# Kernel optimization log

Measured on AMD Instinct MI355X. Metric: run time of the kernel, lower is better.

Reference implementation:

```python
import jax, jax.numpy as jnp
import numpy as np
jax.config.update("jax_enable_x64", True)

N_ITER = 5
B, N = 64, 128

_C1 = jnp.uint64(0x9E3779B97F4A7C15)
_C2 = jnp.uint64(0xBF58476D1CE4E5B9)
_C3 = jnp.uint64(0x94D049BB133111EB)
_SALT = jnp.uint64(0xD1B54A32D192ED03)


def _mix(x):
    # splitmix64 finalizer: a bijection on uint64 -> preserves label equality classes
    z = x + _C1
    z = (z ^ (z >> jnp.uint64(30))) * _C2
    z = (z ^ (z >> jnp.uint64(27))) * _C3
    return z ^ (z >> jnp.uint64(31))


def setup_inputs() -> dict:
    key = jax.random.key(0)
    k1, k2 = jax.random.split(key)
    u = jax.random.uniform(k1, (B, N, N))
    adj = jnp.where(u < 0.06, 1.0, 0.0).astype(jnp.float32)
    adj = jnp.maximum(adj, jnp.transpose(adj, (0, 2, 1)))  # symmetric
    eye = jnp.eye(N, dtype=jnp.float32)
    adj = adj * (1.0 - eye)  # no self loops
    labels = jax.random.randint(k2, (B, N), 0, 10, dtype=jnp.int32)
    return {"adj": adj, "labels": labels}


def _kernel_contrib(h):
    # h: [B, N] uint64 labels. K[i,j] = #{(u,v): label_u == label_v}
    L = h.reshape(-1)                                   # [T]
    eq = (L[:, None] == L[None, :]).astype(jnp.float32)  # [T, T]
    return eq.reshape(B, N, B, N).sum(axis=(1, 3))       # [B, B]


def reference(adj, labels):
    adj_u = (adj > 0.5).astype(jnp.uint64)        # [B, N, N]
    h = _mix(labels.astype(jnp.uint64))           # initial labels (bijective relabel)
    K = _kernel_contrib(h)
    for _ in range(N_ITER):
        # commutative multiset hash of neighbor labels
        nsum = jnp.einsum('bij,bj->bi', adj_u, _mix(h ^ _SALT))
        # combine own label with neighbor multiset -> WL relabel
        h = _mix(_mix(h) + nsum)
        K = K + _kernel_contrib(h)
    d = jnp.sqrt(jnp.diag(K))
    return K / (d[:, None] * d[None, :])
```

## Files before the change

### kernel.cpp

```cpp
#include <hip/hip_runtime.h>

typedef unsigned long long u64;
typedef unsigned int u32;

#define NB 64
#define NN 128
#define NITER 5
#define NGEN 6
#define SALT 0xD1B54A32D192ED03ULL
#define NPAIR_OFF (NB*(NB-1)/2)
#define TSLOTS 256

__device__ __forceinline__ u64 mix64(u64 x) {
    u64 z = x + 0x9E3779B97F4A7C15ULL;
    z = (z ^ (z >> 30)) * 0xBF58476D1CE4E5B9ULL;
    z = (z ^ (z >> 27)) * 0x94D049BB133111EBULL;
    return z ^ (z >> 31);
}

__device__ __forceinline__ void tab_insert(ulonglong2* tab, u64 key) {
    u32 s = (u32)key & (TSLOTS - 1);
    for (;;) {
        u64 old = atomicCAS((unsigned long long*)&tab[s].x, 0ULL, key);
        if (old == 0ULL || old == key) {
            atomicAdd((unsigned long long*)&tab[s].y, 1ULL);
            return;
        }
        s = (s + 1) & (TSLOTS - 1);
    }
}

__global__ __launch_bounds__(512) void wl_propagate(const float* __restrict__ adj,
                                                    const int* __restrict__ labels,
                                                    u64* __restrict__ hgen,
                                                    ulonglong2* __restrict__ tabg,
                                                    float* __restrict__ Kdiag,
                                                    float* __restrict__ out) {
    const int b = blockIdx.x;
    const int t = threadIdx.x;
    const int wave = t >> 6;
    const int lane = t & 63;

    __shared__ u64 bits_sh[NN][2];
    __shared__ u64 h_sh[NN];
    __shared__ u64 g_sh[NN];
    __shared__ u64 psum[4][NN];
    __shared__ ulonglong2 tab[NGEN][TSLOTS];
    __shared__ u32 part[8];

    const float* abase = adj + (size_t)b * NN * NN;
    #pragma unroll
    for (int k = 0; k < 16; ++k) {
        const int row = wave * 16 + k;
        const float* arow = abase + (size_t)row * NN;
        u64 m0 = __ballot(arow[lane] > 0.5f);
        u64 m1 = __ballot(arow[64 + lane] > 0.5f);
        if (lane == 0) { bits_sh[row][0] = m0; bits_sh[row][1] = m1; }
    }

    {
        ulonglong2* tf = &tab[0][0];
        #pragma unroll
        for (int k = 0; k < 3; ++k) tf[t + 512 * k] = make_ulonglong2(0ULL, 0ULL);
    }

    if (t < NN) {
        u64 h = mix64((u64)(unsigned)labels[b * NN + t]);
        h_sh[t] = h;
        hgen[(size_t)b * (NGEN * NN) + t] = h;
    }
    __syncthreads();

    if (t < NN) tab_insert(tab[0], h_sh[t]);

    for (int it = 0; it < NITER; ++it) {
        if (t < NN) g_sh[t] = mix64(h_sh[t] ^ SALT);
        __syncthreads();
        {
            const int i = t & 127;
            const int q = t >> 7;
            u32 m = (u32)(bits_sh[i][q >> 1] >> ((q & 1) * 32));
            const u64* gp = g_sh + q * 32;
            u64 s = 0;
            while (m) {
                int j = __builtin_ctz(m);
                m &= m - 1;
                s += gp[j];
            }
            psum[q][i] = s;
        }
        __syncthreads();
        if (t < NN) {
            u64 hn = mix64(mix64(h_sh[t]) + psum[0][t] + psum[1][t] + psum[2][t] + psum[3][t]);
            h_sh[t] = hn;
            hgen[(size_t)b * (NGEN * NN) + (it + 1) * NN + t] = hn;
            tab_insert(tab[it + 1], hn);
        }
        __syncthreads();
    }

    {
        const ulonglong2* tf = &tab[0][0];
        ulonglong2* tg = tabg + (size_t)b * (NGEN * TSLOTS);
        u32 acc = 0;
        #pragma unroll
        for (int k = 0; k < 3; ++k) {
            const ulonglong2 v = tf[t + 512 * k];
            tg[t + 512 * k] = v;
            const u32 c = (u32)v.y;
            acc += c * c;
        }
        #pragma unroll
        for (int off = 32; off > 0; off >>= 1) acc += __shfl_down(acc, off);
        if (lane == 0) part[wave] = acc;
        __syncthreads();
        if (t == 0) {
            u32 d = 0;
            #pragma unroll
            for (int w = 0; w < 8; ++w) d += part[w];
            Kdiag[b] = (float)d;
            out[b * NB + b] = 1.0f;
        }
    }
}

__global__ __launch_bounds__(256) void wl_pairs(const u64* __restrict__ hgen,
                                                const ulonglong2* __restrict__ tabg,
                                                const float* __restrict__ Kdiag,
                                                float* __restrict__ out) {
    const int p = blockIdx.x;
    int b1 = (int)((1.0f + sqrtf(1.0f + 8.0f * (float)p)) * 0.5f);
    while (b1 * (b1 - 1) / 2 > p) --b1;
    while ((b1 + 1) * b1 / 2 <= p) ++b1;
    const int b2 = p - b1 * (b1 - 1) / 2;

    const int t = threadIdx.x;
    __shared__ ulonglong2 tab[NGEN * TSLOTS];

    {
        const ulonglong2* src = tabg + (size_t)b2 * (NGEN * TSLOTS);
        #pragma unroll
        for (int k = 0; k < 6; ++k) tab[t + 256 * k] = src[t + 256 * k];
    }
    __syncthreads();

    u32 cnt = 0;
    const u64* abase = hgen + (size_t)b1 * (NGEN * NN);
    #pragma unroll
    for (int k = 0; k < 3; ++k) {
        const int idx = t + 256 * k;
        const u64 a = abase[idx];
        const ulonglong2* tg = tab + (idx >> 7) * TSLOTS;
        u32 s = (u32)a & (TSLOTS - 1);
        for (;;) {
            const ulonglong2 v = tg[s];
            if (v.x == a) { cnt += (u32)v.y; break; }
            if (v.x == 0ULL) break;
            s = (s + 1) & (TSLOTS - 1);
        }
    }

    #pragma unroll
    for (int off = 32; off > 0; off >>= 1) cnt += __shfl_down(cnt, off);
    __shared__ u32 part[4];
    if ((t & 63) == 0) part[t >> 6] = cnt;
    __syncthreads();
    if (t == 0) {
        const float v = (float)(part[0] + part[1] + part[2] + part[3])
                      / (sqrtf(Kdiag[b1]) * sqrtf(Kdiag[b2]));
        out[b1 * NB + b2] = v;
        out[b2 * NB + b1] = v;
    }
}

extern "C" void kernel_launch(void* const* d_in, const int* in_sizes, int n_in,
                              void* d_out, int out_size, void* d_ws, size_t ws_size,
                              hipStream_t stream) {
    const float* adj   = (const float*)d_in[0];
    const int*  labels = (const int*)d_in[1];
    float* out = (float*)d_out;

    char* ws = (char*)d_ws;
    u64*        hgen  = (u64*)ws;
    float*      Kdiag = (float*)(ws + 448 * 1024);
    ulonglong2* tabg  = (ulonglong2*)(ws + 512 * 1024);

    wl_propagate<<<NB, 512, 0, stream>>>(adj, labels, hgen, tabg, Kdiag, out);
    wl_pairs<<<NPAIR_OFF, 256, 0, stream>>>(hgen, tabg, Kdiag, out);
}
```

Before: 32.33 us.

## Split hash-table building into separate kernel and shrink per-block state

Hash-table construction moves out of the propagation kernel into a new wl_tables kernel that runs one block per (graph, generation), so tables are built in parallel instead of serially inside each iteration. The propagation kernel now keeps the adjacency bitmask and the label in registers, using float4 loads instead of ballots, and drops one barrier per iteration. Table layout becomes separate key and 32-bit count arrays, so the pair kernel copies less data into shared memory. The cost is an extra kernel launch, a global round-trip for hgen, and a Kdiag accumulated with atomics.

After: 27.96 us. 1.16x faster.

```diff
diff --git a/kernel.cpp b/kernel.cpp
--- a/kernel.cpp
+++ b/kernel.cpp
@@ -18,115 +18,100 @@
     return z ^ (z >> 31);
 }
 
-__device__ __forceinline__ void tab_insert(ulonglong2* tab, u64 key) {
-    u32 s = (u32)key & (TSLOTS - 1);
-    for (;;) {
-        u64 old = atomicCAS((unsigned long long*)&tab[s].x, 0ULL, key);
-        if (old == 0ULL || old == key) {
-            atomicAdd((unsigned long long*)&tab[s].y, 1ULL);
-            return;
-        }
-        s = (s + 1) & (TSLOTS - 1);
-    }
-}
-
-__global__ __launch_bounds__(512) void wl_propagate(const float* __restrict__ adj,
-                                                    const int* __restrict__ labels,
-                                                    u64* __restrict__ hgen,
-                                                    ulonglong2* __restrict__ tabg,
-                                                    float* __restrict__ Kdiag,
-                                                    float* __restrict__ out) {
+__global__ __launch_bounds__(512) void wl_iter(const float* __restrict__ adj,
+                                               const int* __restrict__ labels,
+                                               u64* __restrict__ hgen,
+                                               u32* __restrict__ KdiagU,
+                                               float* __restrict__ out) {
     const int b = blockIdx.x;
     const int t = threadIdx.x;
-    const int wave = t >> 6;
-    const int lane = t & 63;
+    const int u = t & 127;
+    const int q = t >> 7;
 
-    __shared__ u64 bits_sh[NN][2];
-    __shared__ u64 h_sh[NN];
-    __shared__ u64 g_sh[NN];
-    __shared__ u64 psum[4][NN];
-    __shared__ ulonglong2 tab[NGEN][TSLOTS];
-    __shared__ u32 part[8];
+    __shared__ u64 gsh[NN];
+    __shared__ u64 psum[3][NN];
 
-    const float* abase = adj + (size_t)b * NN * NN;
+    const float* rowp = adj + ((size_t)b * NN + u) * NN + q * 32;
+    u32 m = 0;
     #pragma unroll
-    for (int k = 0; k < 16; ++k) {
-        const int row = wave * 16 + k;
-        const float* arow = abase + (size_t)row * NN;
-        u64 m0 = __ballot(arow[lane] > 0.5f);
-        u64 m1 = __ballot(arow[64 + lane] > 0.5f);
-        if (lane == 0) { bits_sh[row][0] = m0; bits_sh[row][1] = m1; }
+    for (int k = 0; k < 8; ++k) {
+        const float4 v = *(const float4*)(rowp + 4 * k);
+        m |= (v.x > 0.5f ? 1u : 0u) << (4 * k);
+        m |= (v.y > 0.5f ? 1u : 0u) << (4 * k + 1);
+        m |= (v.z > 0.5f ? 1u : 0u) << (4 * k + 2);
+        m |= (v.w > 0.5f ? 1u : 0u) << (4 * k + 3);
     }
 
-    {
-        ulonglong2* tf = &tab[0][0];
-        #pragma unroll
-        for (int k = 0; k < 3; ++k) tf[t + 512 * k] = make_ulonglong2(0ULL, 0ULL);
+    u64 h = 0;
+    if (q == 0) {
+        h = mix64((u64)(u32)labels[b * NN + u]);
+        hgen[((size_t)b * NGEN) * NN + u] = h;
+        if (u == 0) out[b * NB + b] = 1.0f;
+        if (u == 1) KdiagU[b] = 0u;
     }
 
-    if (t < NN) {
-        u64 h = mix64((u64)(unsigned)labels[b * NN + t]);
-        h_sh[t] = h;
-        hgen[(size_t)b * (NGEN * NN) + t] = h;
-    }
-    __syncthreads();
-
-    if (t < NN) tab_insert(tab[0], h_sh[t]);
-
     for (int it = 0; it < NITER; ++it) {
-        if (t < NN) g_sh[t] = mix64(h_sh[t] ^ SALT);
+        if (q == 0) gsh[u] = mix64(h ^ SALT);
         __syncthreads();
+        u64 s = 0;
         {
-            const int i = t & 127;
-            const int q = t >> 7;
-            u32 m = (u32)(bits_sh[i][q >> 1] >> ((q & 1) * 32));
-            const u64* gp = g_sh + q * 32;
-            u64 s = 0;
-            while (m) {
-                int j = __builtin_ctz(m);
-                m &= m - 1;
-                s += gp[j];
-            }
-            psum[q][i] = s;
+            u32 mm = m;
+            const u64* gp = gsh + q * 32;
+            while (mm) { int j = __builtin_ctz(mm); mm &= mm - 1; s += gp[j]; }
         }
+        if (q) psum[q - 1][u] = s;
         __syncthreads();
-        if (t < NN) {
-            u64 hn = mix64(mix64(h_sh[t]) + psum[0][t] + psum[1][t] + psum[2][t] + psum[3][t]);
-            h_sh[t] = hn;
-            hgen[(size_t)b * (NGEN * NN) + (it + 1) * NN + t] = hn;
-            tab_insert(tab[it + 1], hn);
-        }
-        __syncthreads();
-    }
-
-    {
-        const ulonglong2* tf = &tab[0][0];
-        ulonglong2* tg = tabg + (size_t)b * (NGEN * TSLOTS);
-        u32 acc = 0;
-        #pragma unroll
-        for (int k = 0; k < 3; ++k) {
-            const ulonglong2 v = tf[t + 512 * k];
-            tg[t + 512 * k] = v;
-            const u32 c = (u32)v.y;
-            acc += c * c;
-        }
-        #pragma unroll
-        for (int off = 32; off > 0; off >>= 1) acc += __shfl_down(acc, off);
-        if (lane == 0) part[wave] = acc;
-        __syncthreads();
-        if (t == 0) {
-            u32 d = 0;
-            #pragma unroll
-            for (int w = 0; w < 8; ++w) d += part[w];
-            Kdiag[b] = (float)d;
-            out[b * NB + b] = 1.0f;
+        if (q == 0) {
+            h = mix64(mix64(h) + s + psum[0][u] + psum[1][u] + psum[2][u]);
+            hgen[((size_t)b * NGEN + (it + 1)) * NN + u] = h;
         }
     }
 }
 
+__global__ __launch_bounds__(128) void wl_tables(const u64* __restrict__ hgen,
+                                                 u64* __restrict__ keysg,
+                                                 u32* __restrict__ cntsg,
+                                                 u32* __restrict__ KdiagU) {
+    const int bg = blockIdx.x;
+    const int t = threadIdx.x;
+
+    __shared__ u64 keys[TSLOTS];
+    __shared__ u32 cnts[TSLOTS];
+    keys[t] = 0ULL; keys[t + 128] = 0ULL;
+    cnts[t] = 0u;   cnts[t + 128] = 0u;
+    __syncthreads();
+
+    const u64 h = hgen[(size_t)bg * NN + t];
+    u32 s = (u32)h & (TSLOTS - 1);
+    for (;;) {
+        u64 old = atomicCAS((unsigned long long*)&keys[s], 0ULL, h);
+        if (old == 0ULL || old == h) { atomicAdd(&cnts[s], 1u); break; }
+        s = (s + 1) & (TSLOTS - 1);
+    }
+    __syncthreads();
+
+    u32 acc;
+    {
+        const u64 k0 = keys[t], k1 = keys[t + 128];
+        const u32 c0 = cnts[t], c1 = cnts[t + 128];
+        keysg[(size_t)bg * TSLOTS + t]       = k0;
+        keysg[(size_t)bg * TSLOTS + t + 128] = k1;
+        cntsg[(size_t)bg * TSLOTS + t]       = c0;
+        cntsg[(size_t)bg * TSLOTS + t + 128] = c1;
+        acc = c0 * c0 + c1 * c1;
+    }
+    #pragma unroll
+    for (int off = 32; off > 0; off >>= 1) acc += __shfl_down(acc, off);
+    __shared__ u32 part[2];
+    if ((t & 63) == 0) part[t >> 6] = acc;
+    __syncthreads();
+    if (t == 0) atomicAdd(&KdiagU[bg / NGEN], part[0] + part[1]);
+}
+
 __global__ __launch_bounds__(256) void wl_pairs(const u64* __restrict__ hgen,
-                                                const ulonglong2* __restrict__ tabg,
-                                                const float* __restrict__ Kdiag,
+                                                const u64* __restrict__ keysg,
+                                                const u32* __restrict__ cntsg,
+                                                const u32* __restrict__ KdiagU,
                                                 float* __restrict__ out) {
     const int p = blockIdx.x;
     int b1 = (int)((1.0f + sqrtf(1.0f + 8.0f * (float)p)) * 0.5f);
@@ -135,39 +120,50 @@
     const int b2 = p - b1 * (b1 - 1) / 2;
 
     const int t = threadIdx.x;
-    __shared__ ulonglong2 tab[NGEN * TSLOTS];
+    __shared__ u64 keys[NGEN * TSLOTS];
+    __shared__ u32 cnts[NGEN * TSLOTS];
 
     {
-        const ulonglong2* src = tabg + (size_t)b2 * (NGEN * TSLOTS);
+        const ulonglong2* src = (const ulonglong2*)(keysg + (size_t)b2 * NGEN * TSLOTS);
+        ulonglong2* dst = (ulonglong2*)keys;
         #pragma unroll
-        for (int k = 0; k < 6; ++k) tab[t + 256 * k] = src[t + 256 * k];
+        for (int k = 0; k < 3; ++k) dst[t + 256 * k] = src[t + 256 * k];
+    }
+    {
+        const uint4* src = (const uint4*)(cntsg + (size_t)b2 * NGEN * TSLOTS);
+        uint4* dst = (uint4*)cnts;
+        #pragma unroll
+        for (int k = 0; k < 2; ++k) {
+            const int idx = t + 256 * k;
+            if (idx < 384) dst[idx] = src[idx];
+        }
     }
     __syncthreads();
 
-    u32 cnt = 0;
-    const u64* abase = hgen + (size_t)b1 * (NGEN * NN);
+    u32 c = 0;
+    const u64* abase = hgen + (size_t)b1 * NGEN * NN;
     #pragma unroll
     for (int k = 0; k < 3; ++k) {
         const int idx = t + 256 * k;
         const u64 a = abase[idx];
-        const ulonglong2* tg = tab + (idx >> 7) * TSLOTS;
+        const int base = (idx >> 7) * TSLOTS;
         u32 s = (u32)a & (TSLOTS - 1);
         for (;;) {
-            const ulonglong2 v = tg[s];
-            if (v.x == a) { cnt += (u32)v.y; break; }
-            if (v.x == 0ULL) break;
+            const u64 kk = keys[base + s];
+            if (kk == a) { c += cnts[base + s]; break; }
+            if (kk == 0ULL) break;
             s = (s + 1) & (TSLOTS - 1);
         }
     }
 
     #pragma unroll
-    for (int off = 32; off > 0; off >>= 1) cnt += __shfl_down(cnt, off);
+    for (int off = 32; off > 0; off >>= 1) c += __shfl_down(c, off);
     __shared__ u32 part[4];
-    if ((t & 63) == 0) part[t >> 6] = cnt;
+    if ((t & 63) == 0) part[t >> 6] = c;
     __syncthreads();
     if (t == 0) {
         const float v = (float)(part[0] + part[1] + part[2] + part[3])
-                      / (sqrtf(Kdiag[b1]) * sqrtf(Kdiag[b2]));
+                      / (sqrtf((float)KdiagU[b1]) * sqrtf((float)KdiagU[b2]));
         out[b1 * NB + b2] = v;
         out[b2 * NB + b1] = v;
     }
@@ -181,10 +177,12 @@
     float* out = (float*)d_out;
 
     char* ws = (char*)d_ws;
-    u64*        hgen  = (u64*)ws;
-    float*      Kdiag = (float*)(ws + 448 * 1024);
-    ulonglong2* tabg  = (ulonglong2*)(ws + 512 * 1024);
+    u64* hgen  = (u64*)ws;
+    u64* keysg = (u64*)(ws + 512 * 1024);
+    u32* cntsg = (u32*)(ws + 1536 * 1024);
+    u32* KdiagU = (u32*)(ws + 2048 * 1024);
 
-    wl_propagate<<<NB, 512, 0, stream>>>(adj, labels, hgen, tabg, Kdiag, out);
-    wl_pairs<<<NPAIR_OFF, 256, 0, stream>>>(hgen, tabg, Kdiag, out);
+    wl_iter  <<<NB, 512, 0, stream>>>(adj, labels, hgen, KdiagU, out);
+    wl_tables<<<NB * NGEN, 128, 0, stream>>>(hgen, keysg, cntsg, KdiagU);
+    wl_pairs <<<NPAIR_OFF, 256, 0, stream>>>(hgen, keysg, cntsg, KdiagU, out);
 }
```
